# Kernel tuning notes

Hardware: AMD Instinct MI355X
Metric: run time of the kernel (lower is better)

Reference implementation:

```python
import jax, jax.numpy as jnp
import numpy as np

B, H, KVH, HD, S = 16, 32, 8, 128, 4096
D = H * HD  # 4096
Q = 1  # decode: one query token per batch element


def rotate_half(x):
    half = x.shape[-1] // 2
    return jnp.concatenate([-x[..., half:], x[..., :half]], axis=-1)


def setup_inputs() -> dict:
    key = jax.random.key(0)
    ks = jax.random.split(key, 8)
    hidden_states = jax.random.normal(ks[0], (B, Q, D), dtype=jnp.float32)
    current_steps = jax.random.randint(ks[1], (B,), 0, S - 1)
    # additive causal mask per batch: positions <= current_step visible
    pos = jnp.arange(S)[None, :]
    attention_mask = jnp.where(pos <= current_steps[:, None], 0.0, -1e9).astype(jnp.float32)[:, None, None, :]  # [B,1,1,S]
    # RoPE cos/sin at each batch element's current position
    inv_freq = 1.0 / (10000.0 ** (jnp.arange(0, HD, 2, dtype=jnp.float32) / HD))
    ang = current_steps[:, None].astype(jnp.float32) * inv_freq[None, :]  # [B, HD/2]
    ang = jnp.concatenate([ang, ang], axis=-1)  # [B, HD]
    cos = jnp.cos(ang)[:, None, None, :]  # [B,1,1,HD]
    sin = jnp.sin(ang)[:, None, None, :]
    past_key = jax.random.normal(ks[2], (B, KVH, S, HD), dtype=jnp.float32)
    past_value = jax.random.normal(ks[3], (B, KVH, S, HD), dtype=jnp.float32)
    sc = 1.0 / np.sqrt(D)
    Wq = jax.random.normal(ks[4], (D, H * HD), dtype=jnp.float32) * sc
    Wk = jax.random.normal(ks[5], (D, KVH * HD), dtype=jnp.float32) * sc
    Wv = jax.random.normal(ks[6], (D, KVH * HD), dtype=jnp.float32) * sc
    Wo = jax.random.normal(ks[7], (H * HD, D), dtype=jnp.float32) * sc
    return dict(hidden_states=hidden_states, attention_mask=attention_mask,
                current_steps=current_steps, cos=cos, sin=sin,
                past_key=past_key, past_value=past_value,
                Wq=Wq, Wk=Wk, Wv=Wv, Wo=Wo)


def reference(hidden_states, attention_mask, current_steps, cos, sin,
              past_key, past_value, Wq, Wk, Wv, Wo):
    b, q_len, d = hidden_states.shape
    # projections -> [B, heads, Q, HD]
    q = (hidden_states @ Wq).reshape(b, q_len, H, HD).transpose(0, 2, 1, 3)
    k = (hidden_states @ Wk).reshape(b, q_len, KVH, HD).transpose(0, 2, 1, 3)
    v = (hidden_states @ Wv).reshape(b, q_len, KVH, HD).transpose(0, 2, 1, 3)
    # RoPE
    q = q * cos + rotate_half(q) * sin
    k = k * cos + rotate_half(k) * sin
    # KV-cache scatter at current_step per batch (slice_scatter equivalent)
    def upd(cache_b, new_b, step):
        return jax.lax.dynamic_update_slice(cache_b, new_b, (0, step, 0))
    new_key = jax.vmap(upd)(past_key, k, current_steps)      # [B,KVH,S,HD]
    new_value = jax.vmap(upd)(past_value, v, current_steps)  # [B,KVH,S,HD]
    # GQA attention
    g = H // KVH
    qg = q.reshape(b, KVH, g, q_len, HD)
    scores = jnp.einsum('bkgqd,bksd->bkgqs', qg, new_key) / np.sqrt(HD)
    scores = scores + attention_mask[:, :, None, :, :]  # [B,1,1,Q,S] broadcast
    probs = jax.nn.softmax(scores, axis=-1)
    out = jnp.einsum('bkgqs,bksd->bkgqd', probs, new_value)
    out = out.reshape(b, H, q_len, HD).transpose(0, 2, 1, 3).reshape(b, q_len, H * HD)
    attn_out = out @ Wo
    return attn_out, new_key, new_value
```

## Files before the change

kernel.cpp:

```cpp
#include <hip/hip_runtime.h>

#define B 16
#define H 32
#define KVH 8
#define HD 128
#define S 4096
#define D 4096
#define NQKV 6144
#define PSPLIT 32
#define WSPLIT 32
#define NCH 16
#define CROWS (S / NCH)
#define SCALE 0.08838834764831845f

typedef float nfloat4 __attribute__((ext_vector_type(4)));

__device__ __forceinline__ float4 ntload4(const float4* p) {
  nfloat4 r = __builtin_nontemporal_load(reinterpret_cast<const nfloat4*>(p));
  return *reinterpret_cast<float4*>(&r);
}
__device__ __forceinline__ void ntstore4(float4* p, float4 v) {
  __builtin_nontemporal_store(*reinterpret_cast<nfloat4*>(&v),
                              reinterpret_cast<nfloat4*>(p));
}
__device__ __forceinline__ float ntloadf(const float* p) {
  return __builtin_nontemporal_load(p);
}

__global__ void k_proj(const float* __restrict__ hs, const float* __restrict__ Wq,
                       const float* __restrict__ Wk, const float* __restrict__ Wv,
                       float* __restrict__ part) {
  int n = blockIdx.x * 256 + threadIdx.x;
  int k0 = blockIdx.y * (D / PSPLIT);
  const float* w; int ldw, col;
  if (n < 4096)      { w = Wq; ldw = 4096; col = n; }
  else if (n < 5120) { w = Wk; ldw = 1024; col = n - 4096; }
  else               { w = Wv; ldw = 1024; col = n - 5120; }
  float acc[B];
#pragma unroll
  for (int b = 0; b < B; b++) acc[b] = 0.f;
  const float* wp = w + (size_t)k0 * ldw + col;
#pragma unroll 8
  for (int k = 0; k < D / PSPLIT; k++) {
    float wv = ntloadf(&wp[(size_t)k * ldw]);
#pragma unroll
    for (int b = 0; b < B; b++) acc[b] = fmaf(hs[b * D + k0 + k], wv, acc[b]);
  }
  float* p = part + (size_t)blockIdx.y * (B * NQKV);
#pragma unroll
  for (int b = 0; b < B; b++) p[(size_t)b * NQKV + n] = acc[b];
}

__global__ void k_reduce_rope(const float* __restrict__ part, const float* __restrict__ cosb,
                              const float* __restrict__ sinb, const int* __restrict__ steps,
                              float* __restrict__ qr, float* __restrict__ nkrow,
                              float* __restrict__ nvrow) {
  int i = blockIdx.x * 256 + threadIdx.x;
  int b = i / 3584, n2 = i % 3584;
  if (n2 < 2560) {
    int hr = n2 >> 6, d = n2 & 63;
    int n_lo = hr * 128 + d, n_hi = n_lo + 64;
    float vlo = 0.f, vhi = 0.f;
#pragma unroll
    for (int c = 0; c < PSPLIT; c++) {
      const float* pc = part + (size_t)c * B * NQKV + (size_t)b * NQKV;
      vlo += ntloadf(&pc[n_lo]);
      vhi += ntloadf(&pc[n_hi]);
    }
    float clo = cosb[b * HD + d], chi = cosb[b * HD + d + 64];
    float slo = sinb[b * HD + d], shi = sinb[b * HD + d + 64];
    float rlo = vlo * clo - vhi * slo;
    float rhi = vhi * chi + vlo * shi;
    if (n_lo < 4096) {
      qr[(size_t)b * D + n_lo] = rlo;
      qr[(size_t)b * D + n_hi] = rhi;
    } else {
      nkrow[(size_t)b * KVH * HD + (n_lo - 4096)] = rlo;
      nkrow[(size_t)b * KVH * HD + (n_hi - 4096)] = rhi;
    }
  } else {
    int j = n2 - 2560;
    float v = 0.f;
#pragma unroll
    for (int c = 0; c < PSPLIT; c++)
      v += ntloadf(&part[(size_t)c * B * NQKV + (size_t)b * NQKV + 5120 + j]);
    nvrow[(size_t)b * KVH * HD + j] = v;
  }
}

__global__ void __launch_bounds__(256)
k_flashKV(const float* __restrict__ pastk, const float* __restrict__ pastv,
          const float* __restrict__ nkrow, const float* __restrict__ nvrow,
          const float* __restrict__ qr, const int* __restrict__ steps,
          float* __restrict__ newk, float* __restrict__ newv,
          float* __restrict__ part, float* __restrict__ stats) {
  int ch = blockIdx.x, kvh = blockIdx.y, b = blockIdx.z;
  int t = threadIdx.x;
  __shared__ float sbuf[CROWS][4];
  __shared__ float redmx[4][4];
  __shared__ float redsm[4][4];
  __shared__ float4 red4[4][4][32];
  int s0 = ch * CROWS;
  int step = steps[b];
  int L = step + 1;
  int h0 = kvh * 4;
  bool any = (s0 < L);
  int w = t >> 6;
  int d4 = t & 31, rr = t >> 5;

  const float4* srcv = (const float4*)(pastv + ((size_t)(b * KVH + kvh) * S + s0) * HD);
  float4*       dstv = (float4*)(newv + ((size_t)(b * KVH + kvh) * S + s0) * HD);
  float4 vsub = ((const float4*)(nvrow + (size_t)(b * KVH + kvh) * HD))[d4];

  {
    int ln = t & 15, rg = t >> 4;
    const float4* qbase = (const float4*)(qr + ((size_t)b * H + h0) * HD);
    float4 q0[4], q1[4];
#pragma unroll
    for (int h = 0; h < 4; h++) {
      q0[h] = qbase[h * 32 + ln];
      q1[h] = qbase[h * 32 + ln + 16];
    }
    const float4* subp = (const float4*)(nkrow + (size_t)(b * KVH + kvh) * HD);
    float4 sub0 = subp[ln], sub1 = subp[ln + 16];
    const float4* src = (const float4*)(pastk + ((size_t)(b * KVH + kvh) * S + s0) * HD);
    float4*       dst = (float4*)(newk + ((size_t)(b * KVH + kvh) * S + s0) * HD);
#pragma unroll 4
    for (int it = 0; it < CROWS / 16; ++it) {
      int row = it * 16 + rg;
      size_t o0 = (size_t)row * 32 + ln;
      float4 k0 = ntload4(&src[o0]);
      float4 k1 = ntload4(&src[o0 + 16]);
      if (s0 + row == step) { k0 = sub0; k1 = sub1; }
      ntstore4(&dst[o0], k0);
      ntstore4(&dst[o0 + 16], k1);
      if (s0 + it * 16 < L) {
        float a0, a1, a2, a3;
        a0 = fmaf(k0.x, q0[0].x, fmaf(k0.y, q0[0].y, fmaf(k0.z, q0[0].z, fmaf(k0.w, q0[0].w,
             fmaf(k1.x, q1[0].x, fmaf(k1.y, q1[0].y, fmaf(k1.z, q1[0].z, k1.w * q1[0].w)))))));
        a1 = fmaf(k0.x, q0[1].x, fmaf(k0.y, q0[1].y, fmaf(k0.z, q0[1].z, fmaf(k0.w, q0[1].w,
             fmaf(k1.x, q1[1].x, fmaf(k1.y, q1[1].y, fmaf(k1.z, q1[1].z, k1.w * q1[1].w)))))));
        a2 = fmaf(k0.x, q0[2].x, fmaf(k0.y, q0[2].y, fmaf(k0.z, q0[2].z, fmaf(k0.w, q0[2].w,
             fmaf(k1.x, q1[2].x, fmaf(k1.y, q1[2].y, fmaf(k1.z, q1[2].z, k1.w * q1[2].w)))))));
        a3 = fmaf(k0.x, q0[3].x, fmaf(k0.y, q0[3].y, fmaf(k0.z, q0[3].z, fmaf(k0.w, q0[3].w,
             fmaf(k1.x, q1[3].x, fmaf(k1.y, q1[3].y, fmaf(k1.z, q1[3].z, k1.w * q1[3].w)))))));
#pragma unroll
        for (int o = 1; o < 16; o <<= 1) {
          a0 += __shfl_xor(a0, o);
          a1 += __shfl_xor(a1, o);
          a2 += __shfl_xor(a2, o);
          a3 += __shfl_xor(a3, o);
        }
        if (ln < 4) {
          float my = (ln == 0) ? a0 : (ln == 1) ? a1 : (ln == 2) ? a2 : a3;
          sbuf[row][ln] = my * SCALE;
        }
      }
    }
  }
  float4 pv0 = ntload4(&srcv[(size_t)rr * 32 + d4]);
  float4 pv1 = ntload4(&srcv[(size_t)(rr + 8) * 32 + d4]);
  __syncthreads();

  bool valid = any && (s0 + t < L);
  float s_0 = valid ? sbuf[t][0] : -1e30f;
  float s_1 = valid ? sbuf[t][1] : -1e30f;
  float s_2 = valid ? sbuf[t][2] : -1e30f;
  float s_3 = valid ? sbuf[t][3] : -1e30f;
  float mx0 = s_0, mx1 = s_1, mx2 = s_2, mx3 = s_3;
#pragma unroll
  for (int o = 1; o < 64; o <<= 1) {
    mx0 = fmaxf(mx0, __shfl_xor(mx0, o));
    mx1 = fmaxf(mx1, __shfl_xor(mx1, o));
    mx2 = fmaxf(mx2, __shfl_xor(mx2, o));
    mx3 = fmaxf(mx3, __shfl_xor(mx3, o));
  }
  if ((t & 63) == 0) { redmx[w][0] = mx0; redmx[w][1] = mx1; redmx[w][2] = mx2; redmx[w][3] = mx3; }
  __syncthreads();
  float m0 = fmaxf(fmaxf(redmx[0][0], redmx[1][0]), fmaxf(redmx[2][0], redmx[3][0]));
  float m1 = fmaxf(fmaxf(redmx[0][1], redmx[1][1]), fmaxf(redmx[2][1], redmx[3][1]));
  float m2 = fmaxf(fmaxf(redmx[0][2], redmx[1][2]), fmaxf(redmx[2][2], redmx[3][2]));
  float m3 = fmaxf(fmaxf(redmx[0][3], redmx[1][3]), fmaxf(redmx[2][3], redmx[3][3]));
  float e0 = valid ? __expf(s_0 - m0) : 0.f;
  float e1 = valid ? __expf(s_1 - m1) : 0.f;
  float e2 = valid ? __expf(s_2 - m2) : 0.f;
  float e3 = valid ? __expf(s_3 - m3) : 0.f;
  float es0 = e0, es1 = e1, es2 = e2, es3 = e3;
#pragma unroll
  for (int o = 1; o < 64; o <<= 1) {
    es0 += __shfl_xor(es0, o);
    es1 += __shfl_xor(es1, o);
    es2 += __shfl_xor(es2, o);
    es3 += __shfl_xor(es3, o);
  }
  if ((t & 63) == 0) { redsm[w][0] = es0; redsm[w][1] = es1; redsm[w][2] = es2; redsm[w][3] = es3; }
  sbuf[t][0] = e0; sbuf[t][1] = e1; sbuf[t][2] = e2; sbuf[t][3] = e3;
  __syncthreads();
  float l0 = redsm[0][0] + redsm[1][0] + redsm[2][0] + redsm[3][0];
  float l1 = redsm[0][1] + redsm[1][1] + redsm[2][1] + redsm[3][1];
  float l2 = redsm[0][2] + redsm[1][2] + redsm[2][2] + redsm[3][2];
  float l3 = redsm[0][3] + redsm[1][3] + redsm[2][3] + redsm[3][3];

  float4 a0 = make_float4(0.f, 0.f, 0.f, 0.f), a1 = a0, a2 = a0, a3 = a0;
#pragma unroll 2
  for (int i = 0; i < CROWS / 16; ++i) {
    int r0 = i * 16 + rr, r1 = r0 + 8;
    float4 v0 = pv0, v1 = pv1;
    if (i + 1 < CROWS / 16) {
      pv0 = ntload4(&srcv[(size_t)(r0 + 16) * 32 + d4]);
      pv1 = ntload4(&srcv[(size_t)(r1 + 16) * 32 + d4]);
    }
    if (s0 + r0 == step) v0 = vsub;
    if (s0 + r1 == step) v1 = vsub;
    ntstore4(&dstv[(size_t)r0 * 32 + d4], v0);
    ntstore4(&dstv[(size_t)r1 * 32 + d4], v1);
    if (any && i * 16 < L - s0) {
      float p00 = sbuf[r0][0], p01 = sbuf[r0][1], p02 = sbuf[r0][2], p03 = sbuf[r0][3];
      float p10 = sbuf[r1][0], p11 = sbuf[r1][1], p12 = sbuf[r1][2], p13 = sbuf[r1][3];
      a0.x = fmaf(p00, v0.x, fmaf(p10, v1.x, a0.x));
      a0.y = fmaf(p00, v0.y, fmaf(p10, v1.y, a0.y));
      a0.z = fmaf(p00, v0.z, fmaf(p10, v1.z, a0.z));
      a0.w = fmaf(p00, v0.w, fmaf(p10, v1.w, a0.w));
      a1.x = fmaf(p01, v0.x, fmaf(p11, v1.x, a1.x));
      a1.y = fmaf(p01, v0.y, fmaf(p11, v1.y, a1.y));
      a1.z = fmaf(p01, v0.z, fmaf(p11, v1.z, a1.z));
      a1.w = fmaf(p01, v0.w, fmaf(p11, v1.w, a1.w));
      a2.x = fmaf(p02, v0.x, fmaf(p12, v1.x, a2.x));
      a2.y = fmaf(p02, v0.y, fmaf(p12, v1.y, a2.y));
      a2.z = fmaf(p02, v0.z, fmaf(p12, v1.z, a2.z));
      a2.w = fmaf(p02, v0.w, fmaf(p12, v1.w, a2.w));
      a3.x = fmaf(p03, v0.x, fmaf(p13, v1.x, a3.x));
      a3.y = fmaf(p03, v0.y, fmaf(p13, v1.y, a3.y));
      a3.z = fmaf(p03, v0.z, fmaf(p13, v1.z, a3.z));
      a3.w = fmaf(p03, v0.w, fmaf(p13, v1.w, a3.w));
    }
  }
  a0.x += __shfl_xor(a0.x, 32); a0.y += __shfl_xor(a0.y, 32);
  a0.z += __shfl_xor(a0.z, 32); a0.w += __shfl_xor(a0.w, 32);
  a1.x += __shfl_xor(a1.x, 32); a1.y += __shfl_xor(a1.y, 32);
  a1.z += __shfl_xor(a1.z, 32); a1.w += __shfl_xor(a1.w, 32);
  a2.x += __shfl_xor(a2.x, 32); a2.y += __shfl_xor(a2.y, 32);
  a2.z += __shfl_xor(a2.z, 32); a2.w += __shfl_xor(a2.w, 32);
  a3.x += __shfl_xor(a3.x, 32); a3.y += __shfl_xor(a3.y, 32);
  a3.z += __shfl_xor(a3.z, 32); a3.w += __shfl_xor(a3.w, 32);
  if ((t & 32) == 0) {
    red4[w][0][d4] = a0; red4[w][1][d4] = a1; red4[w][2][d4] = a2; red4[w][3][d4] = a3;
  }
  __syncthreads();
  if (t < 128) {
    int hh = t >> 5, dd = t & 31;
    float4 x0 = red4[0][hh][dd], x1 = red4[1][hh][dd], x2 = red4[2][hh][dd], x3 = red4[3][hh][dd];
    float4 s;
    s.x = (x0.x + x1.x) + (x2.x + x3.x);
    s.y = (x0.y + x1.y) + (x2.y + x3.y);
    s.z = (x0.z + x1.z) + (x2.z + x3.z);
    s.w = (x0.w + x1.w) + (x2.w + x3.w);
    ((float4*)(part + (((size_t)ch * B + b) * KVH + kvh) * 512))[t] = s;
  }
  if (t == 0) {
    size_t si = (((size_t)ch * B + b) * KVH + kvh) * 8;
    stats[si + 0] = m0; stats[si + 1] = l0;
    stats[si + 2] = m1; stats[si + 3] = l1;
    stats[si + 4] = m2; stats[si + 5] = l2;
    stats[si + 6] = m3; stats[si + 7] = l3;
  }
}

__global__ void k_reduce_ctx(const float* __restrict__ part, const float* __restrict__ stats,
                             float* __restrict__ ctx) {
  int i = blockIdx.x * 256 + threadIdx.x;
  int b = i >> 12, r = i & 4095, h = r >> 7, d = r & 127;
  int kvh = h >> 2, hl = h & 3;
  float M = -1e30f;
#pragma unroll
  for (int c = 0; c < NCH; c++)
    M = fmaxf(M, stats[(((size_t)c * B + b) * KVH + kvh) * 8 + hl * 2]);
  float num = 0.f, den = 0.f;
#pragma unroll
  for (int c = 0; c < NCH; c++) {
    size_t si = (((size_t)c * B + b) * KVH + kvh) * 8 + hl * 2;
    float wgt = __expf(stats[si] - M);
    den += wgt * stats[si + 1];
    num += wgt * part[(((size_t)c * B + b) * KVH + kvh) * 512 + hl * 128 + d];
  }
  ctx[i] = num / den;
}

__global__ void k_wo(const float* __restrict__ ctx, const float* __restrict__ Wo,
                     float* __restrict__ part) {
  int n = blockIdx.x * 256 + threadIdx.x;
  int k0 = blockIdx.y * (D / WSPLIT);
  float acc[B];
#pragma unroll
  for (int b = 0; b < B; b++) acc[b] = 0.f;
  const float* wp = Wo + (size_t)k0 * D + n;
#pragma unroll 8
  for (int k = 0; k < D / WSPLIT; k++) {
    float wv = ntloadf(&wp[(size_t)k * D]);
#pragma unroll
    for (int b = 0; b < B; b++) acc[b] = fmaf(ctx[b * D + k0 + k], wv, acc[b]);
  }
  float* p = part + (size_t)blockIdx.y * (B * D);
#pragma unroll
  for (int b = 0; b < B; b++) p[(size_t)b * D + n] = acc[b];
}

__global__ void k_reduce_out(const float* __restrict__ part, float* __restrict__ out) {
  int i = blockIdx.x * 256 + threadIdx.x;
  float s = 0.f;
#pragma unroll
  for (int c = 0; c < WSPLIT; c++) s += part[(size_t)c * B * D + i];
  out[i] = s;
}

extern "C" void kernel_launch(void* const* d_in, const int* in_sizes, int n_in,
                              void* d_out, int out_size, void* d_ws, size_t ws_size,
                              hipStream_t stream) {
  const float* hs    = (const float*)d_in[0];
  const int*   steps = (const int*)d_in[2];
  const float* cosb  = (const float*)d_in[3];
  const float* sinb  = (const float*)d_in[4];
  const float* pk    = (const float*)d_in[5];
  const float* pvv   = (const float*)d_in[6];
  const float* Wq    = (const float*)d_in[7];
  const float* Wk    = (const float*)d_in[8];
  const float* Wv    = (const float*)d_in[9];
  const float* Wo    = (const float*)d_in[10];

  float* attn_out = (float*)d_out;
  float* newk = attn_out + (size_t)B * D;
  float* newv = newk + (size_t)B * KVH * S * HD;

  float* ws = (float*)d_ws;
  float* A        = ws;
  float* p_part   = A;
  float* p_wopart = A;
  float* p_pvpart = A + 3145728;
  float* p_stats  = p_pvpart + 1048576;
  float* p_qr     = p_stats + 16384;
  float* p_nkrow  = p_qr + (size_t)B * D;
  float* p_nvrow  = p_nkrow + (size_t)B * KVH * HD;
  float* p_ctx    = p_nvrow + (size_t)B * KVH * HD;

  hipLaunchKernelGGL(k_proj, dim3(NQKV / 256, PSPLIT), dim3(256), 0, stream,
                     hs, Wq, Wk, Wv, p_part);
  hipLaunchKernelGGL(k_reduce_rope, dim3(B * 3584 / 256), dim3(256), 0, stream,
                     p_part, cosb, sinb, steps, p_qr, p_nkrow, p_nvrow);
  hipLaunchKernelGGL(k_flashKV, dim3(NCH, KVH, B), dim3(256), 0, stream,
                     pk, pvv, p_nkrow, p_nvrow, p_qr, steps, newk, newv,
                     p_pvpart, p_stats);
  hipLaunchKernelGGL(k_reduce_ctx, dim3(B * D / 256), dim3(256), 0, stream,
                     p_pvpart, p_stats, p_ctx);
  hipLaunchKernelGGL(k_wo, dim3(D / 256, WSPLIT), dim3(256), 0, stream,
                     p_ctx, Wo, p_wopart);
  hipLaunchKernelGGL(k_reduce_out, dim3(B * D / 256), dim3(256), 0, stream,
                     p_wopart, attn_out);
}
```

Before: 303.4 us.

## Stage activations transposed in LDS for GEMV kernels, use regular KV stores

The projection and output GEMV kernels now stage the 16-batch activation slice into shared memory, transposed so each k step reads four float4 values instead of 16 scalar global loads. The new KV cache rows are written with ordinary stores instead of nontemporal stores, and the partial-sum reads in the reduction kernels switch to nontemporal loads. This aims to cut redundant global or L1 traffic for activations in the weight-streaming kernels and to adjust cache behaviour for the large KV copy. It adds a __syncthreads and shared-memory use per block, and the changed store policy could add cache pollution during the KV copy.

```diff
diff --git a/kernel.cpp b/kernel.cpp
--- a/kernel.cpp
+++ b/kernel.cpp
@@ -19,10 +19,6 @@
   nfloat4 r = __builtin_nontemporal_load(reinterpret_cast<const nfloat4*>(p));
   return *reinterpret_cast<float4*>(&r);
 }
-__device__ __forceinline__ void ntstore4(float4* p, float4 v) {
-  __builtin_nontemporal_store(*reinterpret_cast<nfloat4*>(&v),
-                              reinterpret_cast<nfloat4*>(p));
-}
 __device__ __forceinline__ float ntloadf(const float* p) {
   return __builtin_nontemporal_load(p);
 }
@@ -30,8 +26,19 @@
 __global__ void k_proj(const float* __restrict__ hs, const float* __restrict__ Wq,
                        const float* __restrict__ Wk, const float* __restrict__ Wv,
                        float* __restrict__ part) {
-  int n = blockIdx.x * 256 + threadIdx.x;
+  __shared__ float4 hsT[D / PSPLIT][4];
+  int t = threadIdx.x;
+  int n = blockIdx.x * 256 + t;
   int k0 = blockIdx.y * (D / PSPLIT);
+#pragma unroll
+  for (int i = 0; i < (D / PSPLIT) * 4 / 256; i++) {
+    int idx = i * 256 + t;
+    int k = idx >> 2, b4 = idx & 3;
+    hsT[k][b4] = make_float4(hs[(size_t)(b4 * 4 + 0) * D + k0 + k],
+                             hs[(size_t)(b4 * 4 + 1) * D + k0 + k],
+                             hs[(size_t)(b4 * 4 + 2) * D + k0 + k],
+                             hs[(size_t)(b4 * 4 + 3) * D + k0 + k]);
+  }
   const float* w; int ldw, col;
   if (n < 4096)      { w = Wq; ldw = 4096; col = n; }
   else if (n < 5120) { w = Wk; ldw = 1024; col = n - 4096; }
@@ -40,11 +47,19 @@
 #pragma unroll
   for (int b = 0; b < B; b++) acc[b] = 0.f;
   const float* wp = w + (size_t)k0 * ldw + col;
-#pragma unroll 8
+  __syncthreads();
+#pragma unroll 4
   for (int k = 0; k < D / PSPLIT; k++) {
     float wv = ntloadf(&wp[(size_t)k * ldw]);
-#pragma unroll
-    for (int b = 0; b < B; b++) acc[b] = fmaf(hs[b * D + k0 + k], wv, acc[b]);
+    float4 h0 = hsT[k][0], h1 = hsT[k][1], h2 = hsT[k][2], h3 = hsT[k][3];
+    acc[0]  = fmaf(h0.x, wv, acc[0]);  acc[1]  = fmaf(h0.y, wv, acc[1]);
+    acc[2]  = fmaf(h0.z, wv, acc[2]);  acc[3]  = fmaf(h0.w, wv, acc[3]);
+    acc[4]  = fmaf(h1.x, wv, acc[4]);  acc[5]  = fmaf(h1.y, wv, acc[5]);
+    acc[6]  = fmaf(h1.z, wv, acc[6]);  acc[7]  = fmaf(h1.w, wv, acc[7]);
+    acc[8]  = fmaf(h2.x, wv, acc[8]);  acc[9]  = fmaf(h2.y, wv, acc[9]);
+    acc[10] = fmaf(h2.z, wv, acc[10]); acc[11] = fmaf(h2.w, wv, acc[11]);
+    acc[12] = fmaf(h3.x, wv, acc[12]); acc[13] = fmaf(h3.y, wv, acc[13]);
+    acc[14] = fmaf(h3.z, wv, acc[14]); acc[15] = fmaf(h3.w, wv, acc[15]);
   }
   float* p = part + (size_t)blockIdx.y * (B * NQKV);
 #pragma unroll
@@ -132,8 +147,8 @@
       float4 k0 = ntload4(&src[o0]);
       float4 k1 = ntload4(&src[o0 + 16]);
       if (s0 + row == step) { k0 = sub0; k1 = sub1; }
-      ntstore4(&dst[o0], k0);
-      ntstore4(&dst[o0 + 16], k1);
+      dst[o0] = k0;
+      dst[o0 + 16] = k1;
       if (s0 + it * 16 < L) {
         float a0, a1, a2, a3;
         a0 = fmaf(k0.x, q0[0].x, fmaf(k0.y, q0[0].y, fmaf(k0.z, q0[0].z, fmaf(k0.w, q0[0].w,
@@ -212,8 +227,8 @@
     }
     if (s0 + r0 == step) v0 = vsub;
     if (s0 + r1 == step) v1 = vsub;
-    ntstore4(&dstv[(size_t)r0 * 32 + d4], v0);
-    ntstore4(&dstv[(size_t)r1 * 32 + d4], v1);
+    dstv[(size_t)r0 * 32 + d4] = v0;
+    dstv[(size_t)r1 * 32 + d4] = v1;
     if (any && i * 16 < L - s0) {
       float p00 = sbuf[r0][0], p01 = sbuf[r0][1], p02 = sbuf[r0][2], p03 = sbuf[r0][3];
       float p10 = sbuf[r1][0], p11 = sbuf[r1][1], p12 = sbuf[r1][2], p13 = sbuf[r1][3];
@@ -281,24 +296,43 @@
     size_t si = (((size_t)c * B + b) * KVH + kvh) * 8 + hl * 2;
     float wgt = __expf(stats[si] - M);
     den += wgt * stats[si + 1];
-    num += wgt * part[(((size_t)c * B + b) * KVH + kvh) * 512 + hl * 128 + d];
+    num += wgt * ntloadf(&part[(((size_t)c * B + b) * KVH + kvh) * 512 + hl * 128 + d]);
   }
   ctx[i] = num / den;
 }
 
 __global__ void k_wo(const float* __restrict__ ctx, const float* __restrict__ Wo,
                      float* __restrict__ part) {
-  int n = blockIdx.x * 256 + threadIdx.x;
+  __shared__ float4 cxT[D / WSPLIT][4];
+  int t = threadIdx.x;
+  int n = blockIdx.x * 256 + t;
   int k0 = blockIdx.y * (D / WSPLIT);
+#pragma unroll
+  for (int i = 0; i < (D / WSPLIT) * 4 / 256; i++) {
+    int idx = i * 256 + t;
+    int k = idx >> 2, b4 = idx & 3;
+    cxT[k][b4] = make_float4(ctx[(size_t)(b4 * 4 + 0) * D + k0 + k],
+                             ctx[(size_t)(b4 * 4 + 1) * D + k0 + k],
+                             ctx[(size_t)(b4 * 4 + 2) * D + k0 + k],
+                             ctx[(size_t)(b4 * 4 + 3) * D + k0 + k]);
+  }
   float acc[B];
 #pragma unroll
   for (int b = 0; b < B; b++) acc[b] = 0.f;
   const float* wp = Wo + (size_t)k0 * D + n;
-#pragma unroll 8
+  __syncthreads();
+#pragma unroll 4
   for (int k = 0; k < D / WSPLIT; k++) {
     float wv = ntloadf(&wp[(size_t)k * D]);
-#pragma unroll
-    for (int b = 0; b < B; b++) acc[b] = fmaf(ctx[b * D + k0 + k], wv, acc[b]);
+    float4 h0 = cxT[k][0], h1 = cxT[k][1], h2 = cxT[k][2], h3 = cxT[k][3];
+    acc[0]  = fmaf(h0.x, wv, acc[0]);  acc[1]  = fmaf(h0.y, wv, acc[1]);
+    acc[2]  = fmaf(h0.z, wv, acc[2]);  acc[3]  = fmaf(h0.w, wv, acc[3]);
+    acc[4]  = fmaf(h1.x, wv, acc[4]);  acc[5]  = fmaf(h1.y, wv, acc[5]);
+    acc[6]  = fmaf(h1.z, wv, acc[6]);  acc[7]  = fmaf(h1.w, wv, acc[7]);
+    acc[8]  = fmaf(h2.x, wv, acc[8]);  acc[9]  = fmaf(h2.y, wv, acc[9]);
+    acc[10] = fmaf(h2.z, wv, acc[10]); acc[11] = fmaf(h2.w, wv, acc[11]);
+    acc[12] = fmaf(h3.x, wv, acc[12]); acc[13] = fmaf(h3.y, wv, acc[13]);
+    acc[14] = fmaf(h3.z, wv, acc[14]); acc[15] = fmaf(h3.w, wv, acc[15]);
   }
   float* p = part + (size_t)blockIdx.y * (B * D);
 #pragma unroll
@@ -309,7 +343,7 @@
   int i = blockIdx.x * 256 + threadIdx.x;
   float s = 0.f;
 #pragma unroll
-  for (int c = 0; c < WSPLIT; c++) s += part[(size_t)c * B * D + i];
+  for (int c = 0; c < WSPLIT; c++) s += ntloadf(&part[(size_t)c * B * D + i]);
   out[i] = s;
 }
 
```

After: 291.2 us. 4.0% less time.
